# Optimization experiments

Measured on AMD Instinct MI355X. Metric: run time of the kernel, lower is better.

## Reference

```python
import jax, jax.numpy as jnp
import numpy as np

DIM = 768
NUM_HEADS = 12
KERNEL = 3
DILATIONS = (1, 2, 3)


def setup_inputs() -> dict:
    key = jax.random.key(0)
    k1, k2, k3, k4 = jax.random.split(key, 4)
    B, N, C = 4, 4096, DIM
    return {
        "x": jax.random.normal(k1, (B, N, C), jnp.float32),
        "w_qkv": jax.random.normal(k2, (3 * C, C), jnp.float32) * 0.02,
        "w_proj": jax.random.normal(k3, (C, C), jnp.float32) * 0.02,
        "b_proj": jax.random.normal(k4, (C,), jnp.float32) * 0.02,
    }


def _dilate_attention(q, k, v, dilation, head_dim, kernel):
    # q,k,v: [B, d, N] where d = C / num_dilation
    B, d, N = q.shape
    h = d // head_dim
    scale = head_dim ** -0.5
    qh = q.reshape(B, h, head_dim, N)
    kh = k.reshape(B, h, head_dim, N)
    vh = v.reshape(B, h, head_dim, N)
    pad = dilation * (kernel - 1) // 2

    def windows(t):
        # gather the `kernel` dilated neighbors along N with zero padding
        tp = jnp.pad(t, ((0, 0), (0, 0), (0, 0), (pad, pad)))
        return jnp.stack([tp[..., j * dilation: j * dilation + N] for j in range(kernel)], axis=3)  # [B,h,hd,kernel,N]

    k_win = windows(kh)
    v_win = windows(vh)
    scores = jnp.einsum('bhdn,bhdkn->bhnk', qh, k_win) * scale  # [B,h,N,kernel]
    # Torch nn.Unfold on the [B,d,N,1] 'image' yields kernel*kernel columns;
    # only the center width-column is real, the rest are zero padding -> score 0.
    kk = kernel * kernel
    center = (kernel - 1) // 2
    scores_full = jnp.zeros(scores.shape[:3] + (kk,), scores.dtype).at[..., center::kernel].set(scores)
    probs = jax.nn.softmax(scores_full, axis=-1)  # zero-key columns dilute the softmax, faithfully
    probs_real = probs[..., center::kernel]  # [B,h,N,kernel]; zero-key columns multiply zero values
    out = jnp.einsum('bhnk,bhdkn->bhnd', probs_real, v_win)  # [B,h,N,hd]
    return out.transpose(0, 2, 1, 3).reshape(B, N, d)


def reference(x, w_qkv, w_proj, b_proj):
    B, N, C = x.shape
    nd = len(DILATIONS)
    head_dim = C // NUM_HEADS
    # [B,N,3C] -> [B,N,3,nd,C/nd] -> [nd,3,B,C/nd,N]
    qkv = (x @ w_qkv.T).reshape(B, N, 3, nd, C // nd).transpose(3, 2, 0, 4, 1)
    outs = [_dilate_attention(qkv[i, 0], qkv[i, 1], qkv[i, 2], DILATIONS[i], head_dim, KERNEL)
            for i in range(nd)]
    xo = jnp.stack(outs, axis=2).reshape(B, N, C)  # [B,N,nd,d] -> [B,N,C]
    xo = xo @ w_proj.T + b_proj
    # matches torch return (x, x2=None, v, k, q); x2 omitted (is_decoder=False)
    return (xo, qkv[:, 2], qkv[:, 1], qkv[:, 0])
```

## Files before the change

### kernel.cpp

```cpp
#include <hip/hip_runtime.h>

typedef __attribute__((ext_vector_type(8))) short bf16x8;
typedef __attribute__((ext_vector_type(4))) float f32x4;

#define SZQKV 12582912

__device__ __forceinline__ unsigned short f2bf(float f) {
    unsigned int u = __float_as_uint(f);
    unsigned int r = (u + 0x7FFFu + ((u >> 16) & 1u)) >> 16;
    return (unsigned short)r;
}

#define GLDS16(g, l) __builtin_amdgcn_global_load_lds( \
    (const __attribute__((address_space(1))) unsigned int*)(g), \
    (__attribute__((address_space(3))) unsigned int*)(l), 16, 0, 0)

__global__ void cast_all(const float* __restrict__ x,
                         const float* __restrict__ wqkv,
                         const float* __restrict__ wproj,
                         unsigned short* __restrict__ dst) {
    const int T1 = 12582912;
    const int T2 = T1 + 1769472;
    const int T3 = T2 + 589824;
    int stride = gridDim.x * blockDim.x * 4;
    for (int base = (blockIdx.x * blockDim.x + threadIdx.x) * 4; base < T3; base += stride) {
        const float* src; int off;
        if (base < T1)      { src = x;     off = base; }
        else if (base < T2) { src = wqkv;  off = base - T1; }
        else                { src = wproj; off = base - T2; }
        float4 v = *(const float4*)(src + off);
        ushort4 o;
        o.x = f2bf(v.x); o.y = f2bf(v.y); o.z = f2bf(v.z); o.w = f2bf(v.w);
        *(ushort4*)(dst + base) = o;
    }
}

template <int MODE>
__global__ __launch_bounds__(512, 2) void gemm_big(const unsigned short* __restrict__ A,
                                                   const unsigned short* __restrict__ Bw,
                                                   const float* __restrict__ bias,
                                                   float* __restrict__ dout,
                                                   int nby) {
    __shared__ unsigned char lds8[73728];
    const int t = threadIdx.x;
    const int lane = t & 63;
    const int w = t >> 6;
    const int wm = w >> 1, wn = w & 1;

    const int cpx = gridDim.x >> 3;
    const int orig = blockIdx.x;
    const int wgid = (orig & 7) * cpx + (orig >> 3);
    const int bx = wgid / nby, by = wgid - bx * nby;
    const int m0 = bx * 256;
    const int n0 = by * 128;

    const unsigned char* Ab = (const unsigned char*)A;
    const unsigned char* Bb = (const unsigned char*)Bw;

    size_t aSrc0, aSrc1, bSrc;
    {
        int c0 = t, c1 = 512 + t;
        int r0 = c0 >> 2, p0 = (c0 & 3) << 4;
        int r1 = c1 >> 2, p1 = (c1 & 3) << 4;
        aSrc0 = (size_t)(m0 + r0) * 1536 + (p0 ^ ((r0 & 3) << 4));
        aSrc1 = (size_t)(m0 + r1) * 1536 + (p1 ^ ((r1 & 3) << 4));
        int rb = t >> 2, pb = (t & 3) << 4;
        bSrc  = (size_t)(n0 + rb) * 1536 + (pb ^ ((rb & 3) << 4));
    }

    int aOff[4], bOff[4];
#pragma unroll
    for (int mi = 0; mi < 4; ++mi) {
        int row = wm * 64 + mi * 16 + (lane & 15);
        aOff[mi] = row * 64 + ((((lane >> 4) << 4)) ^ ((row & 3) << 4));
    }
#pragma unroll
    for (int ni = 0; ni < 4; ++ni) {
        int row = wn * 64 + ni * 16 + (lane & 15);
        bOff[ni] = 16384 + row * 64 + ((((lane >> 4) << 4)) ^ ((row & 3) << 4));
    }

    f32x4 acc[4][4] = {};

#define STAGE(bi, kt) do { \
    unsigned char* dst_ = lds8 + (bi) * 24576; \
    GLDS16(Ab + aSrc0 + (size_t)(kt) * 64, dst_ + t * 16); \
    GLDS16(Ab + aSrc1 + (size_t)(kt) * 64, dst_ + 8192 + t * 16); \
    GLDS16(Bb + bSrc  + (size_t)(kt) * 64, dst_ + 16384 + t * 16); \
} while (0)

    STAGE(0, 0);
    STAGE(1, 1);
    int bi = 0;
    for (int kt = 0; kt < 24; ++kt) {
        if (kt < 22) {
            int si = bi + 2; if (si >= 3) si -= 3;
            STAGE(si, kt + 2);
            asm volatile("s_waitcnt vmcnt(6)" ::: "memory");
        } else if (kt == 22) {
            asm volatile("s_waitcnt vmcnt(3)" ::: "memory");
        } else {
            asm volatile("s_waitcnt vmcnt(0)" ::: "memory");
        }
        __builtin_amdgcn_s_barrier();
        asm volatile("" ::: "memory");
        const unsigned char* base = lds8 + bi * 24576;
        bf16x8 av[4], bv[4];
#pragma unroll
        for (int mi = 0; mi < 4; ++mi) av[mi] = *(const bf16x8*)(base + aOff[mi]);
#pragma unroll
        for (int ni = 0; ni < 4; ++ni) bv[ni] = *(const bf16x8*)(base + bOff[ni]);
#pragma unroll
        for (int mi = 0; mi < 4; ++mi)
#pragma unroll
            for (int ni = 0; ni < 4; ++ni)
                acc[mi][ni] = __builtin_amdgcn_mfma_f32_16x16x32_bf16(av[mi], bv[ni], acc[mi][ni], 0, 0, 0);
        asm volatile("s_waitcnt lgkmcnt(0)" ::: "memory");
        __builtin_amdgcn_s_barrier();
        asm volatile("" ::: "memory");
        ++bi; if (bi == 3) bi = 0;
    }
#undef STAGE

    const int crow = (lane >> 4) * 4;
    const int ccol = lane & 15;
    if (MODE == 0) {
        const int b = m0 >> 12;
        const int n_base = m0 & 4095;
#pragma unroll
        for (int mi = 0; mi < 4; ++mi) {
            int n = n_base + wm * 64 + mi * 16 + crow;
#pragma unroll
            for (int ni = 0; ni < 4; ++ni) {
                int o = n0 + wn * 64 + ni * 16 + ccol;
                int sel = o / 768;
                int rem = o - sel * 768;
                float* dst = dout + (size_t)(3 - sel) * SZQKV
                           + ((size_t)((rem >> 8) * 4 + b) * 256 + (rem & 255)) * 4096 + n;
                *(f32x4*)dst = acc[mi][ni];
            }
        }
    } else {
#pragma unroll
        for (int mi = 0; mi < 4; ++mi) {
            int m = m0 + wm * 64 + mi * 16 + crow;
#pragma unroll
            for (int ni = 0; ni < 4; ++ni) {
                int o = n0 + wn * 64 + ni * 16 + ccol;
                float bb = bias[o];
#pragma unroll
                for (int r = 0; r < 4; ++r)
                    dout[(size_t)(m + r) * 768 + o] = acc[mi][ni][r] + bb;
            }
        }
    }
}

__global__ __launch_bounds__(256) void attn_kernel(const float* __restrict__ qkv,
                                                   unsigned short* __restrict__ attnbf) {
    const int chunk = blockIdx.x;
    const int dil_i = blockIdx.y;
    const int b     = blockIdx.z;
    const int dil   = dil_i + 1;
    const int t  = threadIdx.x;
    const int h  = t >> 6;
    const int nl = t & 63;
    const int n  = chunk * 64 + nl;

    const size_t gb = (size_t)(dil_i * 4 + b) * 256 * 4096;
    const float* Q = qkv + (size_t)3 * SZQKV + gb;
    const float* K = qkv + (size_t)2 * SZQKV + gb;
    const float* V = qkv + (size_t)1 * SZQKV + gb;

    const int nm = n - dil, np = n + dil;
    const bool vm = (nm >= 0), vp = (np < 4096);
    const int nmc = vm ? nm : 0, npc = vp ? np : 4095;

    float s0 = 0.f, s1 = 0.f, s2 = 0.f;
    {
        const float* qrow = Q + (size_t)h * 64 * 4096;
        const float* krow = K + (size_t)h * 64 * 4096;
        for (int d = 0; d < 64; ++d) {
            float q = qrow[n];
            s0 += q * krow[nmc];
            s1 += q * krow[n];
            s2 += q * krow[npc];
            qrow += 4096; krow += 4096;
        }
    }
    s0 = vm ? s0 * 0.125f : 0.f;
    s1 *= 0.125f;
    s2 = vp ? s2 * 0.125f : 0.f;
    float mx = fmaxf(0.f, fmaxf(s0, fmaxf(s1, s2)));
    float e0 = __expf(s0 - mx), e1 = __expf(s1 - mx), e2 = __expf(s2 - mx);
    float den = e0 + e1 + e2 + 6.f * __expf(-mx);
    float inv = 1.f / den;
    float p0 = vm ? e0 * inv : 0.f;
    float p1 = e1 * inv;
    float p2 = vp ? e2 * inv : 0.f;

    __shared__ unsigned short lout[256][65];
    {
        const float* vrow = V + (size_t)h * 64 * 4096;
        for (int d = 0; d < 64; ++d) {
            float o = p0 * vrow[nmc] + p1 * vrow[n] + p2 * vrow[npc];
            lout[h * 64 + d][nl] = f2bf(o);
            vrow += 4096;
        }
    }
    __syncthreads();

#pragma unroll
    for (int i = 0; i < 8; ++i) {
        int linear = i * 256 + t;
        int nn   = linear >> 5;
        int cblk = linear & 31;
        union { unsigned short u[8]; f32x4 v; } tt;
#pragma unroll
        for (int j = 0; j < 8; ++j) tt.u[j] = lout[cblk * 8 + j][nn];
        unsigned short* dst = attnbf + (size_t)(b * 4096 + chunk * 64 + nn) * 768
                            + dil_i * 256 + cblk * 8;
        *(f32x4*)dst = tt.v;
    }
}

extern "C" void kernel_launch(void* const* d_in, const int* in_sizes, int n_in,
                              void* d_out, int out_size, void* d_ws, size_t ws_size,
                              hipStream_t stream) {
    const float* x     = (const float*)d_in[0];
    const float* wqkv  = (const float*)d_in[1];
    const float* wproj = (const float*)d_in[2];
    const float* bproj = (const float*)d_in[3];
    float* out = (float*)d_out;

    unsigned short* xbf     = (unsigned short*)d_ws;
    unsigned short* wqkvbf  = xbf + 12582912;
    unsigned short* wprojbf = wqkvbf + 1769472;
    unsigned short* attnbf  = wprojbf + 589824;

    cast_all<<<2048, 256, 0, stream>>>(x, wqkv, wproj, xbf);

    gemm_big<0><<<dim3(64 * 18), 512, 0, stream>>>(xbf, wqkvbf, nullptr, out, 18);

    attn_kernel<<<dim3(64, 3, 4), 256, 0, stream>>>(out, attnbf);

    gemm_big<1><<<dim3(64 * 6), 512, 0, stream>>>(attnbf, wprojbf, bproj, out, 6);
}
```

Measured before the change: 173.0 us.

## Enlarge GEMM tiles to 256x256 with K=64 double buffering and setprio

Both GEMMs now use 256x256 output tiles instead of 256x128. Each of the 8 waves computes a 128x64 sub-tile, and each K step is 64 wide with two LDS buffers instead of 32 wide with three. The LDS swizzle becomes an 8-way XOR pattern, and s_setprio is raised around the MFMA bursts. The aim is higher arithmetic intensity and fewer barriers per FLOP. In exchange, LDS per block grows to 128KB, accumulator registers double, and there are fewer blocks (576 and 192), which may hurt occupancy and wave balance across CUs.

```diff
diff --git a/kernel.cpp b/kernel.cpp
--- a/kernel.cpp
+++ b/kernel.cpp
@@ -36,91 +36,101 @@
 }
 
 template <int MODE>
-__global__ __launch_bounds__(512, 2) void gemm_big(const unsigned short* __restrict__ A,
-                                                   const unsigned short* __restrict__ Bw,
-                                                   const float* __restrict__ bias,
-                                                   float* __restrict__ dout,
-                                                   int nby) {
-    __shared__ unsigned char lds8[73728];
+__global__ __launch_bounds__(512, 2) void gemm8(const unsigned short* __restrict__ A,
+                                                const unsigned short* __restrict__ Bw,
+                                                const float* __restrict__ bias,
+                                                float* __restrict__ dout,
+                                                int nby) {
+    __shared__ unsigned char lds8[131072];
     const int t = threadIdx.x;
     const int lane = t & 63;
     const int w = t >> 6;
-    const int wm = w >> 1, wn = w & 1;
+    const int wm = w >> 2;
+    const int wn = w & 3;
 
     const int cpx = gridDim.x >> 3;
     const int orig = blockIdx.x;
     const int wgid = (orig & 7) * cpx + (orig >> 3);
     const int bx = wgid / nby, by = wgid - bx * nby;
     const int m0 = bx * 256;
-    const int n0 = by * 128;
+    const int n0 = by * 256;
 
     const unsigned char* Ab = (const unsigned char*)A;
     const unsigned char* Bb = (const unsigned char*)Bw;
 
-    size_t aSrc0, aSrc1, bSrc;
-    {
-        int c0 = t, c1 = 512 + t;
-        int r0 = c0 >> 2, p0 = (c0 & 3) << 4;
-        int r1 = c1 >> 2, p1 = (c1 & 3) << 4;
-        aSrc0 = (size_t)(m0 + r0) * 1536 + (p0 ^ ((r0 & 3) << 4));
-        aSrc1 = (size_t)(m0 + r1) * 1536 + (p1 ^ ((r1 & 3) << 4));
-        int rb = t >> 2, pb = (t & 3) << 4;
-        bSrc  = (size_t)(n0 + rb) * 1536 + (pb ^ ((rb & 3) << 4));
-    }
-
-    int aOff[4], bOff[4];
-#pragma unroll
-    for (int mi = 0; mi < 4; ++mi) {
-        int row = wm * 64 + mi * 16 + (lane & 15);
-        aOff[mi] = row * 64 + ((((lane >> 4) << 4)) ^ ((row & 3) << 4));
-    }
-#pragma unroll
-    for (int ni = 0; ni < 4; ++ni) {
-        int row = wn * 64 + ni * 16 + (lane & 15);
-        bOff[ni] = 16384 + row * 64 + ((((lane >> 4) << 4)) ^ ((row & 3) << 4));
-    }
-
-    f32x4 acc[4][4] = {};
-
-#define STAGE(bi, kt) do { \
-    unsigned char* dst_ = lds8 + (bi) * 24576; \
-    GLDS16(Ab + aSrc0 + (size_t)(kt) * 64, dst_ + t * 16); \
-    GLDS16(Ab + aSrc1 + (size_t)(kt) * 64, dst_ + 8192 + t * 16); \
-    GLDS16(Bb + bSrc  + (size_t)(kt) * 64, dst_ + 16384 + t * 16); \
+    const int trow = t >> 3;
+    const int jx = ((t & 7) ^ (trow & 7)) << 4;
+    const size_t aBase = (size_t)(m0 + trow) * 1536 + jx;
+    const size_t bBase = (size_t)(n0 + trow) * 1536 + jx;
+    const int ldst = t * 16;
+
+    const int rA = wm * 128 + (lane & 15);
+    const int rB = wn * 64 + (lane & 15);
+    const int xt0 = (((lane >> 4)) ^ (lane & 7)) << 4;
+    const int xt1 = ((4 + (lane >> 4)) ^ (lane & 7)) << 4;
+
+    f32x4 acc[8][4] = {};
+
+#define STAGE(kt, bsel) do { \
+    unsigned char* db_ = lds8 + (bsel) * 65536; \
+    const size_t ko_ = (size_t)(kt) * 128; \
+    GLDS16(Ab + aBase + ko_,          db_ + ldst); \
+    GLDS16(Ab + aBase + ko_ + 98304,  db_ + ldst + 8192); \
+    GLDS16(Ab + aBase + ko_ + 196608, db_ + ldst + 16384); \
+    GLDS16(Ab + aBase + ko_ + 294912, db_ + ldst + 24576); \
+    GLDS16(Bb + bBase + ko_,          db_ + 32768 + ldst); \
+    GLDS16(Bb + bBase + ko_ + 98304,  db_ + 32768 + ldst + 8192); \
+    GLDS16(Bb + bBase + ko_ + 196608, db_ + 32768 + ldst + 16384); \
+    GLDS16(Bb + bBase + ko_ + 294912, db_ + 32768 + ldst + 24576); \
+} while (0)
+
+#define LDA4(base_, xt_) do { \
+    _Pragma("unroll") \
+    for (int mi = 0; mi < 4; ++mi) \
+        av[mi] = *(const bf16x8*)(bufA + (rA + (base_) + mi * 16) * 128 + (xt_)); \
+} while (0)
+
+#define LDB4(xt_) do { \
+    _Pragma("unroll") \
+    for (int ni = 0; ni < 4; ++ni) \
+        bv[ni] = *(const bf16x8*)(bufB + (rB + ni * 16) * 128 + (xt_)); \
+} while (0)
+
+#define MM(rbase_) do { \
+    __builtin_amdgcn_s_setprio(1); \
+    _Pragma("unroll") \
+    for (int mi = 0; mi < 4; ++mi) \
+    _Pragma("unroll") \
+    for (int ni = 0; ni < 4; ++ni) \
+        acc[(rbase_) + mi][ni] = __builtin_amdgcn_mfma_f32_16x16x32_bf16(av[mi], bv[ni], acc[(rbase_) + mi][ni], 0, 0, 0); \
+    __builtin_amdgcn_s_setprio(0); \
 } while (0)
 
     STAGE(0, 0);
-    STAGE(1, 1);
-    int bi = 0;
-    for (int kt = 0; kt < 24; ++kt) {
-        if (kt < 22) {
-            int si = bi + 2; if (si >= 3) si -= 3;
-            STAGE(si, kt + 2);
-            asm volatile("s_waitcnt vmcnt(6)" ::: "memory");
-        } else if (kt == 22) {
-            asm volatile("s_waitcnt vmcnt(3)" ::: "memory");
+    for (int kt = 0; kt < 12; ++kt) {
+        if (kt < 11) {
+            STAGE(kt + 1, (kt + 1) & 1);
+            asm volatile("s_waitcnt vmcnt(8)" ::: "memory");
         } else {
             asm volatile("s_waitcnt vmcnt(0)" ::: "memory");
         }
         __builtin_amdgcn_s_barrier();
         asm volatile("" ::: "memory");
-        const unsigned char* base = lds8 + bi * 24576;
+        const unsigned char* bufA = lds8 + (kt & 1) * 65536;
+        const unsigned char* bufB = bufA + 32768;
         bf16x8 av[4], bv[4];
-#pragma unroll
-        for (int mi = 0; mi < 4; ++mi) av[mi] = *(const bf16x8*)(base + aOff[mi]);
-#pragma unroll
-        for (int ni = 0; ni < 4; ++ni) bv[ni] = *(const bf16x8*)(base + bOff[ni]);
-#pragma unroll
-        for (int mi = 0; mi < 4; ++mi)
-#pragma unroll
-            for (int ni = 0; ni < 4; ++ni)
-                acc[mi][ni] = __builtin_amdgcn_mfma_f32_16x16x32_bf16(av[mi], bv[ni], acc[mi][ni], 0, 0, 0);
+        LDA4(0, xt0); LDB4(xt0); MM(0);
+        LDA4(64, xt0); MM(4);
+        LDA4(0, xt1); LDB4(xt1); MM(0);
+        LDA4(64, xt1); MM(4);
         asm volatile("s_waitcnt lgkmcnt(0)" ::: "memory");
         __builtin_amdgcn_s_barrier();
         asm volatile("" ::: "memory");
-        ++bi; if (bi == 3) bi = 0;
     }
 #undef STAGE
+#undef LDA4
+#undef LDB4
+#undef MM
 
     const int crow = (lane >> 4) * 4;
     const int ccol = lane & 15;
@@ -128,8 +138,8 @@
         const int b = m0 >> 12;
         const int n_base = m0 & 4095;
 #pragma unroll
-        for (int mi = 0; mi < 4; ++mi) {
-            int n = n_base + wm * 64 + mi * 16 + crow;
+        for (int mi = 0; mi < 8; ++mi) {
+            int n = n_base + wm * 128 + mi * 16 + crow;
 #pragma unroll
             for (int ni = 0; ni < 4; ++ni) {
                 int o = n0 + wn * 64 + ni * 16 + ccol;
@@ -142,8 +152,8 @@
         }
     } else {
 #pragma unroll
-        for (int mi = 0; mi < 4; ++mi) {
-            int m = m0 + wm * 64 + mi * 16 + crow;
+        for (int mi = 0; mi < 8; ++mi) {
+            int m = m0 + wm * 128 + mi * 16 + crow;
 #pragma unroll
             for (int ni = 0; ni < 4; ++ni) {
                 int o = n0 + wn * 64 + ni * 16 + ccol;
@@ -240,9 +250,9 @@
 
     cast_all<<<2048, 256, 0, stream>>>(x, wqkv, wproj, xbf);
 
-    gemm_big<0><<<dim3(64 * 18), 512, 0, stream>>>(xbf, wqkvbf, nullptr, out, 18);
+    gemm8<0><<<dim3(576), 512, 0, stream>>>(xbf, wqkvbf, nullptr, out, 9);
 
     attn_kernel<<<dim3(64, 3, 4), 256, 0, stream>>>(out, attnbf);
 
-    gemm_big<1><<<dim3(64 * 6), 512, 0, stream>>>(attnbf, wprojbf, bproj, out, 6);
-}
+    gemm8<1><<<dim3(192), 512, 0, stream>>>(attnbf, wprojbf, bproj, out, 3);
+}
```

New measurement: 178.8 us. 1.03x slower.

## Replace projection GEMM with 128x128-tile triple-buffered kernel and LDS-staged epilogue

Applied to the files above, without the earlier changes.

Adds a dedicated output-projection GEMM that uses 128x128 tiles with 256 threads, giving 768 workgroups where the old launch had 384. It keeps a three-stage global-to-LDS pipeline with XOR-swizzled layouts and remaps block IDs across XCDs. The epilogue stages accumulators through LDS so the bias add and fp32 stores are coalesced 16-byte writes. The aim is better occupancy and CU fill for the small N=768 GEMM and cheaper output writes, at the cost of less data reuse per tile.

```diff
diff --git a/kernel.cpp b/kernel.cpp
--- a/kernel.cpp
+++ b/kernel.cpp
@@ -156,6 +156,120 @@
     }
 }
 
+__global__ __launch_bounds__(256, 3) void gemm_proj128(const unsigned short* __restrict__ A,
+                                                       const unsigned short* __restrict__ Bw,
+                                                       const float* __restrict__ bias,
+                                                       float* __restrict__ dout) {
+    __shared__ unsigned char lds8[49152];
+    const int t = threadIdx.x;
+    const int lane = t & 63;
+    const int w = t >> 6;
+    const int wm = w >> 1, wn = w & 1;
+
+    const int cpx = gridDim.x >> 3;
+    const int orig = blockIdx.x;
+    const int wgid = (orig & 7) * cpx + (orig >> 3);
+    const int bx = wgid / 6, by = wgid - bx * 6;
+    const int m0 = bx * 128, n0 = by * 128;
+
+    const unsigned char* Ab = (const unsigned char*)A;
+    const unsigned char* Bb = (const unsigned char*)Bw;
+
+    const int srow = t >> 2;
+    const int sc = ((t & 3) ^ (srow & 3)) << 4;
+    const size_t aBase = (size_t)(m0 + srow) * 1536 + sc;
+    const size_t bBase = (size_t)(n0 + srow) * 1536 + sc;
+    const int ldst = t * 16;
+
+    const int rA = wm * 64 + (lane & 15);
+    const int rB = wn * 64 + (lane & 15);
+    const int xt = (((lane >> 4)) ^ (lane & 3)) << 4;
+
+    f32x4 acc[4][4] = {};
+
+#define STAGE(kt, bi) do { \
+    unsigned char* db_ = lds8 + (bi) * 16384; \
+    const size_t ko_ = (size_t)(kt) * 64; \
+    GLDS16(Ab + aBase + ko_,         db_ + ldst); \
+    GLDS16(Ab + aBase + ko_ + 98304, db_ + ldst + 4096); \
+    GLDS16(Bb + bBase + ko_,         db_ + 8192 + ldst); \
+    GLDS16(Bb + bBase + ko_ + 98304, db_ + 8192 + ldst + 4096); \
+} while (0)
+
+    STAGE(0, 0);
+    STAGE(1, 1);
+    int bi = 0;
+    for (int kt = 0; kt < 24; ++kt) {
+        if (kt < 22) {
+            int si = bi + 2; if (si >= 3) si -= 3;
+            STAGE(kt + 2, si);
+            asm volatile("s_waitcnt vmcnt(8)" ::: "memory");
+        } else if (kt == 22) {
+            asm volatile("s_waitcnt vmcnt(4)" ::: "memory");
+        } else {
+            asm volatile("s_waitcnt vmcnt(0)" ::: "memory");
+        }
+        __builtin_amdgcn_s_barrier();
+        asm volatile("" ::: "memory");
+        const unsigned char* bufA = lds8 + bi * 16384;
+        const unsigned char* bufB = bufA + 8192;
+        bf16x8 av[4], bv[4];
+#pragma unroll
+        for (int mi = 0; mi < 4; ++mi)
+            av[mi] = *(const bf16x8*)(bufA + (rA + mi * 16) * 64 + xt);
+#pragma unroll
+        for (int ni = 0; ni < 4; ++ni)
+            bv[ni] = *(const bf16x8*)(bufB + (rB + ni * 16) * 64 + xt);
+#pragma unroll
+        for (int mi = 0; mi < 4; ++mi)
+#pragma unroll
+            for (int ni = 0; ni < 4; ++ni)
+                acc[mi][ni] = __builtin_amdgcn_mfma_f32_16x16x32_bf16(av[mi], bv[ni], acc[mi][ni], 0, 0, 0);
+        asm volatile("s_waitcnt lgkmcnt(0)" ::: "memory");
+        __builtin_amdgcn_s_barrier();
+        asm volatile("" ::: "memory");
+        ++bi; if (bi == 3) bi = 0;
+    }
+#undef STAGE
+
+    float* ldsf = (float*)lds8;
+    const int ccol = lane & 15;
+    const int hi4 = (lane >> 4) * 4;
+#pragma unroll
+    for (int s = 0; s < 2; ++s) {
+        if (wm == s) {
+#pragma unroll
+            for (int mi = 0; mi < 4; ++mi)
+#pragma unroll
+                for (int ni = 0; ni < 4; ++ni) {
+                    int o = wn * 64 + ni * 16 + ccol;
+                    int m2b = mi * 16 + hi4;
+#pragma unroll
+                    for (int r = 0; r < 4; ++r)
+                        ldsf[(m2b + r) * 128 + (o ^ (((m2b + r) & 7) << 2))] = acc[mi][ni][r];
+                }
+        }
+        asm volatile("s_waitcnt lgkmcnt(0)" ::: "memory");
+        __builtin_amdgcn_s_barrier();
+        asm volatile("" ::: "memory");
+#pragma unroll
+        for (int it = 0; it < 8; ++it) {
+            int idx = it * 256 + t;
+            int row = idx >> 5;
+            int c4 = (idx & 31) * 4;
+            f32x4 v = *(const f32x4*)&ldsf[row * 128 + (c4 ^ ((row & 7) << 2))];
+            f32x4 b4 = *(const f32x4*)(bias + n0 + c4);
+            v = v + b4;
+            float* dst = dout + (size_t)(m0 + s * 64 + row) * 768 + n0 + c4;
+            *(f32x4*)dst = v;
+        }
+        if (s == 0) {
+            __builtin_amdgcn_s_barrier();
+            asm volatile("" ::: "memory");
+        }
+    }
+}
+
 __global__ __launch_bounds__(256) void attn_kernel(const float* __restrict__ qkv,
                                                    unsigned short* __restrict__ attnbf) {
     const int chunk = blockIdx.x;
@@ -244,5 +358,5 @@
 
     attn_kernel<<<dim3(64, 3, 4), 256, 0, stream>>>(out, attnbf);
 
-    gemm_big<1><<<dim3(64 * 6), 512, 0, stream>>>(attnbf, wprojbf, bproj, out, 6);
-}
+    gemm_proj128<<<dim3(768), 256, 0, stream>>>(attnbf, wprojbf, bproj, out);
+}
```

Measured after the change: 174.7 us. About the same (+1.0%).
